# Optimization experiments

Measured on AMD Instinct MI355X. Metric: run time of the kernel, lower is better.

The kernel has to match this reference:

```python
import jax, jax.numpy as jnp
import numpy as np

T, B, H, I = 128, 32, 256, 256


def setup_inputs() -> dict:
    key = jax.random.key(0)
    ks = jax.random.split(key, 8)
    s = 0.05
    embs = jax.random.normal(ks[0], (T, B, I), jnp.float32)
    lens = jax.random.randint(ks[1], (B,), 1, T + 1)  # lengths in [1, T]
    W_ih = jax.random.normal(ks[2], (4 * H, I), jnp.float32) * s
    W_hh = jax.random.normal(ks[3], (4 * H, H), jnp.float32) * s
    b_ih = jax.random.normal(ks[4], (4 * H,), jnp.float32) * s
    b_hh = jax.random.normal(ks[5], (4 * H,), jnp.float32) * s
    W_a = jax.random.normal(ks[6], (H, 2 * H), jnp.float32) * s  # attention combine (Luong-style)
    b_a = jax.random.normal(ks[7], (H,), jnp.float32) * s
    return {"embs": embs, "lens": lens, "W_ih": W_ih, "W_hh": W_hh,
            "b_ih": b_ih, "b_hh": b_hh, "W_a": W_a, "b_a": b_a}


def reference(embs, lens, W_ih, W_hh, b_ih, b_hh, W_a, b_a):
    Tn, Bn, _ = embs.shape
    Hn = W_hh.shape[1]
    t_idx = jnp.arange(Tn)

    def step(carry, inp):
        h, c, buf, h_fin, c_fin = carry  # h,c: [B,H]; buf: [T,B,H] history of outputs
        t, emb = inp
        # dot-product attention of current hidden over past outputs (steps < t)
        scores = jnp.einsum('tbh,bh->tb', buf, h)
        valid = (t_idx < t)[:, None]
        alpha = jax.nn.softmax(jnp.where(valid, scores, -1e9), axis=0)
        ctx = jnp.einsum('tb,tbh->bh', alpha, buf)
        h_att = jnp.tanh(jnp.concatenate([ctx, h], axis=-1) @ W_a.T + b_a)
        h = jnp.where(t > 0, h_att, h)  # no history at t=0
        # standard PyTorch LSTM cell (gate order i,f,g,o)
        gates = emb @ W_ih.T + b_ih + h @ W_hh.T + b_hh
        i_g, f_g, g_g, o_g = jnp.split(gates, 4, axis=-1)
        c = jax.nn.sigmoid(f_g) * c + jax.nn.sigmoid(i_g) * jnp.tanh(g_g)
        h = jax.nn.sigmoid(o_g) * jnp.tanh(c)
        buf = buf.at[t].set(h)
        take = (t == lens - 1)[:, None]
        h_fin = jnp.where(take, h, h_fin)
        c_fin = jnp.where(take, c, c_fin)
        return (h, c, buf, h_fin, c_fin), h

    z = jnp.zeros((Bn, Hn), embs.dtype)
    buf0 = jnp.zeros((Tn, Bn, Hn), embs.dtype)
    carry, output = jax.lax.scan(step, (z, z, buf0, z, z), (t_idx, embs))
    # output: [T,B,H]; final (h,c) gathered at t == lens-1: [B,H]
    return output, carry[3], carry[4]
```

## Files before the change

### kernel.cpp

```cpp
#include <hip/hip_runtime.h>


#define T_DIM 128
#define B_DIM 32

typedef _Float16 half2_t __attribute__((ext_vector_type(2)));

static __device__ __forceinline__ unsigned pack2(float a, float b) {
  half2_t h;
  h.x = (_Float16)a;
  h.y = (_Float16)b;
  return __builtin_bit_cast(unsigned, h);
}

static __device__ __forceinline__ float dot2f(unsigned w, unsigned v, float acc) {
  half2_t a = __builtin_bit_cast(half2_t, w);
  half2_t b = __builtin_bit_cast(half2_t, v);
#if __has_builtin(__builtin_amdgcn_fdot2)
  return __builtin_amdgcn_fdot2(a, b, acc, false);
#else
  return acc + (float)a.x * (float)b.x + (float)a.y * (float)b.y;
#endif
}

static __device__ __forceinline__ float dot8(uint4 w, uint4 v, float acc) {
  acc = dot2f(w.x, v.x, acc);
  acc = dot2f(w.y, v.y, acc);
  acc = dot2f(w.z, v.z, acc);
  acc = dot2f(w.w, v.w, acc);
  return acc;
}

static __device__ __forceinline__ float lo16(unsigned u) {
  return (float)__builtin_bit_cast(half2_t, u).x;
}
static __device__ __forceinline__ float hi16(unsigned u) {
  return (float)__builtin_bit_cast(half2_t, u).y;
}

static __device__ __forceinline__ float fsig(float x) {
  return __builtin_amdgcn_rcpf(1.f + __expf(-x));
}
static __device__ __forceinline__ float ftanh(float x) {
  float e = __expf(2.f * x);
  return 1.f - 2.f * __builtin_amdgcn_rcpf(e + 1.f);
}

__global__ void pack_weights(const float* __restrict__ W_ih, const float* __restrict__ W_hh,
                             const float* __restrict__ W_a, float* __restrict__ W_ihT,
                             uint4* __restrict__ Whh_pack, uint4* __restrict__ Wa_pack,
                             unsigned long long* __restrict__ ywp,
                             unsigned long long* __restrict__ hx) {
  int n = blockIdx.x * 256 + threadIdx.x;
  {
    int k = n >> 10, r = n & 1023;
    W_ihT[n] = W_ih[r * 256 + k];
  }
  if (n < 32768) {
    int m = n >> 12, tid = (n >> 3) & 511, i = n & 7;
    int r_local = tid >> 2, qk = tid & 3;
    int q = r_local >> 5, jl = r_local & 31;
    int r = q * 256 + m * 32 + jl;
    const float* src = W_hh + r * 256 + (4 * i + qk) * 8;
    uint4 v;
    v.x = pack2(src[0], src[1]);
    v.y = pack2(src[2], src[3]);
    v.z = pack2(src[4], src[5]);
    v.w = pack2(src[6], src[7]);
    Whh_pack[n] = v;
  }
  if (n < 16384) {
    int m = n >> 11, thr = (n >> 2) & 511, c = n & 3;
    int j = thr >> 1, type = thr & 1;
    int col0 = type * 256 + m * 32 + c * 8;
    const float* src = W_a + j * 512 + col0;
    uint4 v;
    v.x = pack2(src[0], src[1]);
    v.y = pack2(src[2], src[3]);
    v.z = pack2(src[4], src[5]);
    v.w = pack2(src[6], src[7]);
    Wa_pack[n] = v;
  }
  if (n < 65536)
    __hip_atomic_store(&ywp[n], 0ull, __ATOMIC_RELAXED, __HIP_MEMORY_SCOPE_AGENT);
  else if (n < 69632)
    __hip_atomic_store(&hx[n - 65536], 0ull, __ATOMIC_RELAXED, __HIP_MEMORY_SCOPE_AGENT);
}

__global__ void compute_gih(const float* __restrict__ embs, const float* __restrict__ W_ihT,
                            const float* __restrict__ b_ih, const float* __restrict__ b_hh,
                            float* __restrict__ gih) {
  __shared__ float embS[8][256];
  const int tid = threadIdx.x;
  const int tb0 = blockIdx.x * 8;
#pragma unroll
  for (int e = 0; e < 8; ++e) embS[e][tid] = embs[(size_t)(tb0 + e) * 256 + tid];
  __syncthreads();
  float acc[8][4];
#pragma unroll
  for (int e = 0; e < 8; ++e)
#pragma unroll
    for (int q = 0; q < 4; ++q) acc[e][q] = 0.f;
  for (int k = 0; k < 256; ++k) {
    float w0 = W_ihT[k * 1024 + tid];
    float w1 = W_ihT[k * 1024 + tid + 256];
    float w2 = W_ihT[k * 1024 + tid + 512];
    float w3 = W_ihT[k * 1024 + tid + 768];
#pragma unroll
    for (int e = 0; e < 8; ++e) {
      float x = embS[e][k];
      acc[e][0] += x * w0;
      acc[e][1] += x * w1;
      acc[e][2] += x * w2;
      acc[e][3] += x * w3;
    }
  }
#pragma unroll
  for (int q = 0; q < 4; ++q) {
    float bias = b_ih[q * 256 + tid] + b_hh[q * 256 + tid];
#pragma unroll
    for (int e = 0; e < 8; ++e)
      gih[(size_t)(tb0 + e) * 1024 + q * 256 + tid] = acc[e][q] + bias;
  }
}

__global__ void __launch_bounds__(512, 1)
alstm_rec(const int* __restrict__ lens, const float* __restrict__ gih,
          const uint4* __restrict__ Whh_pack, const uint4* __restrict__ Wa_pack,
          const float* __restrict__ b_a, unsigned long long* __restrict__ hx,
          unsigned long long* __restrict__ ywp, float* __restrict__ out,
          float* __restrict__ hfin, float* __restrict__ cfin) {
  const int tid = threadIdx.x;
  const int b = blockIdx.x & 31;
  const int m = blockIdx.x >> 5;

  __shared__ __align__(16) unsigned histS[16384];
  __shared__ __align__(16) unsigned ystoreS[16384];
  __shared__ __align__(16) unsigned h2[128];
  __shared__ __align__(16) unsigned hp2[128];
  __shared__ __align__(16) unsigned hsl2[16];
  __shared__ float sc[128];
  __shared__ float zpartF[4][256];
  __shared__ float gsl[128];

  uint4 wh4[8];
  {
    const uint4* p = Whh_pack + ((size_t)m * 512 + tid) * 8;
#pragma unroll
    for (int i = 0; i < 8; ++i) wh4[i] = p[i];
  }
  uint4 wa4[4];
  {
    const uint4* p = Wa_pack + ((size_t)m * 512 + tid) * 4;
#pragma unroll
    for (int i = 0; i < 4; ++i) wa4[i] = p[i];
  }
  const float ba_j = (tid < 256) ? b_a[tid] : 0.f;
  const int len_b = lens[b];
  const int r_local = tid >> 2, qk = tid & 3;
  const int gq = r_local >> 5, gjl = r_local & 31;

  if (tid < 128) hp2[tid] = 0u;
  float c_reg = 0.f;
  __syncthreads();

  for (int t = 0; t < T_DIM; ++t) {
    float gih_v = gih[((size_t)t * 32 + b) * 1024 + gq * 256 + m * 32 + gjl];
    float w_j = 0.f;

    if (t > 0) {
      if (tid < 256) {
        const unsigned long long* base = ywp + b * 2048 + tid;
        unsigned long long v[8];
        for (;;) {
          bool ok = true;
#pragma unroll
          for (int mm = 0; mm < 8; ++mm)
            v[mm] = __hip_atomic_load(base + mm * 256, __ATOMIC_RELAXED, __HIP_MEMORY_SCOPE_AGENT);
#pragma unroll
          for (int mm = 0; mm < 8; ++mm) ok &= ((unsigned)v[mm] == (unsigned)t);
          if (ok) break;
          __builtin_amdgcn_s_sleep(1);
        }
        float y = 0.f, w = 0.f;
#pragma unroll
        for (int mm = 0; mm < 8; ++mm) {
          unsigned pl = (unsigned)(v[mm] >> 32);
          y += lo16(pl);
          w += hi16(pl);
        }
        w_j = w;
        float yn = __shfl_xor(y, 1);
        if (!(tid & 1)) {
          const int p = tid >> 1, sx = (t - 1) & 31;
          ystoreS[(t - 1) * 128 + ((((p >> 2) ^ sx) << 2) | (p & 3))] = pack2(y, yn);
        }
      } else if (tid < 384) {
        const int p = tid - 256;
        unsigned long long v;
        for (;;) {
          v = __hip_atomic_load(&hx[b * 128 + p], __ATOMIC_RELAXED, __HIP_MEMORY_SCOPE_AGENT);
          if ((unsigned)v == (unsigned)t) break;
          __builtin_amdgcn_s_sleep(1);
        }
        unsigned pair = (unsigned)(v >> 32);
        h2[p] = pair;
        histS[(t - 1) * 128 + ((((p >> 2) ^ ((t - 1) & 31)) << 2) | (p & 3))] = pair;
      }
      __syncthreads();
      {
        const int s = tid >> 2, part = tid & 3;
        float a = 0.f;
        if (s < t) {
          const int sx = s & 31;
#pragma unroll
          for (int i = 0; i < 8; ++i) {
            const int c = 4 * i + part;
            uint4 hv = *(const uint4*)&histS[s * 128 + ((c ^ sx) << 2)];
            uint4 qv = *(const uint4*)&h2[c << 2];
            a = dot8(hv, qv, a);
          }
        }
        a += __shfl_xor(a, 1);
        a += __shfl_xor(a, 2);
        if (part == 0 && s < t) sc[s] = a;
      }
      __syncthreads();
      if (tid < 64) {
        float v0 = (tid < t) ? sc[tid] : -3.0e38f;
        float v1 = (tid + 64 < t) ? sc[tid + 64] : -3.0e38f;
        float mx = fmaxf(v0, v1);
#pragma unroll
        for (int off = 32; off >= 1; off >>= 1) mx = fmaxf(mx, __shfl_xor(mx, off));
        float e0 = (tid < t) ? __expf(v0 - mx) : 0.f;
        float e1 = (tid + 64 < t) ? __expf(v1 - mx) : 0.f;
        float sm = e0 + e1;
#pragma unroll
        for (int off = 32; off >= 1; off >>= 1) sm += __shfl_xor(sm, off);
        float inv = __builtin_amdgcn_rcpf(sm);
        sc[tid] = e0 * inv;
        sc[tid + 64] = e1 * inv;
      }
      __syncthreads();
      {
        const int sp = tid >> 7, p2 = tid & 127;
        float c0 = 0.f, c1 = 0.f;
        for (int s = sp; s < t; s += 4) {
          float al = sc[s];
          unsigned yv = ystoreS[s * 128 + ((((p2 >> 2) ^ (s & 31)) << 2) | (p2 & 3))];
          c0 += al * lo16(yv);
          c1 += al * hi16(yv);
        }
        zpartF[sp][2 * p2] = c0;
        zpartF[sp][2 * p2 + 1] = c1;
      }
      __syncthreads();
      if (tid < 256) {
        float z = zpartF[0][tid] + zpartF[1][tid] + zpartF[2][tid] + zpartF[3][tid];
        float hv = ftanh(ba_j + w_j + z);
        float o = __shfl_xor(hv, 1);
        if (!(tid & 1)) hp2[tid >> 1] = pack2(hv, o);
      }
      __syncthreads();
    }
    {
      float a = 0.f;
#pragma unroll
      for (int i = 0; i < 8; ++i) {
        const int c = 4 * i + qk;
        uint4 hv = *(const uint4*)&hp2[c << 2];
        a = dot8(wh4[i], hv, a);
      }
      a += __shfl_xor(a, 1);
      a += __shfl_xor(a, 2);
      if (qk == 0) gsl[r_local] = a + gih_v;
    }
    __syncthreads();
    if (tid < 32) {
      float ig = fsig(gsl[tid]);
      float fg = fsig(gsl[32 + tid]);
      float gg = ftanh(gsl[64 + tid]);
      float og = fsig(gsl[96 + tid]);
      float cn = fg * c_reg + ig * gg;
      float hn = og * ftanh(cn);
      c_reg = cn;
      out[((size_t)t * 32 + b) * 256 + m * 32 + tid] = hn;
      if (t == len_b - 1) {
        hfin[b * 256 + m * 32 + tid] = hn;
        cfin[b * 256 + m * 32 + tid] = cn;
      }
      float o = __shfl_xor(hn, 1);
      if (!(tid & 1)) {
        unsigned u = pack2(hn, o);
        hsl2[tid >> 1] = u;
        unsigned long long v =
            ((unsigned long long)u << 32) | (unsigned long long)(unsigned)(t + 1);
        __hip_atomic_store(&hx[b * 128 + m * 16 + (tid >> 1)], v, __ATOMIC_RELAXED,
                           __HIP_MEMORY_SCOPE_AGENT);
      }
    }
    __syncthreads();
    {
      float acc = 0.f;
#pragma unroll
      for (int c = 0; c < 4; ++c) {
        uint4 hv = *(const uint4*)&hsl2[c * 4];
        acc = dot8(wa4[c], hv, acc);
      }
      float other = __shfl_xor(acc, 1);
      if (!(tid & 1)) {
        unsigned long long v = ((unsigned long long)pack2(acc, other) << 32) |
                               (unsigned long long)(unsigned)(t + 1);
        __hip_atomic_store(&ywp[b * 2048 + m * 256 + (tid >> 1)], v, __ATOMIC_RELAXED,
                           __HIP_MEMORY_SCOPE_AGENT);
      }
    }
  }
}

extern "C" void kernel_launch(void* const* d_in, const int* in_sizes, int n_in,
                              void* d_out, int out_size, void* d_ws, size_t ws_size,
                              hipStream_t stream) {
  const float* embs = (const float*)d_in[0];
  const int* lens = (const int*)d_in[1];
  const float* W_ih = (const float*)d_in[2];
  const float* W_hh = (const float*)d_in[3];
  const float* b_ih = (const float*)d_in[4];
  const float* b_hh = (const float*)d_in[5];
  const float* W_a = (const float*)d_in[6];
  const float* b_a = (const float*)d_in[7];

  float* out = (float*)d_out;
  float* hfin = out + (size_t)T_DIM * B_DIM * 256;
  float* cfin = hfin + (size_t)B_DIM * 256;

  char* ws = (char*)d_ws;
  float* gih = (float*)ws;
  float* W_ihT = (float*)(ws + 16777216);
  uint4* Whh_pack = (uint4*)(ws + 17825792);
  uint4* Wa_pack = (uint4*)(ws + 18350080);
  unsigned long long* ywp = (unsigned long long*)(ws + 18612224);
  unsigned long long* hx = (unsigned long long*)(ws + 19136512);

  pack_weights<<<1024, 256, 0, stream>>>(W_ih, W_hh, W_a, W_ihT, Whh_pack, Wa_pack, ywp, hx);
  compute_gih<<<512, 256, 0, stream>>>(embs, W_ihT, b_ih, b_hh, gih);
  alstm_rec<<<256, 512, 0, stream>>>(lens, gih, Whh_pack, Wa_pack, b_a, hx, ywp, out, hfin,
                                     cfin);
}
```

Baseline: 623.3 us.

## Distribute attention scores across column-slice blocks and exchange partial scores

Each block now keeps only its own 32-column slice of the hidden history and computes partial attention scores against all past steps for that slice, publishing them through a global flag-tagged buffer. Consumers sum the eight partials instead of gathering the full hidden vector and recomputing full dot products over the whole history. The y projection history is kept in fp32 shared memory, and the W_a projection work is remapped so one thread computes both the y and w halves for a row. The aim is to cut shared-memory traffic and the per-step score loop, at the cost of a different cross-block exchange pattern and an extra barrier.

```diff
diff --git a/kernel.cpp b/kernel.cpp
--- a/kernel.cpp
+++ b/kernel.cpp
@@ -50,7 +50,7 @@
                              const float* __restrict__ W_a, float* __restrict__ W_ihT,
                              uint4* __restrict__ Whh_pack, uint4* __restrict__ Wa_pack,
                              unsigned long long* __restrict__ ywp,
-                             unsigned long long* __restrict__ hx) {
+                             unsigned long long* __restrict__ psx) {
   int n = blockIdx.x * 256 + threadIdx.x;
   {
     int k = n >> 10, r = n & 1023;
@@ -70,9 +70,8 @@
     Whh_pack[n] = v;
   }
   if (n < 16384) {
-    int m = n >> 11, thr = (n >> 2) & 511, c = n & 3;
-    int j = thr >> 1, type = thr & 1;
-    int col0 = type * 256 + m * 32 + c * 8;
+    int m = n >> 11, j = (n >> 3) & 255, c = n & 7;
+    int col0 = (c < 4) ? (m * 32 + c * 8) : (256 + m * 32 + (c - 4) * 8);
     const float* src = W_a + j * 512 + col0;
     uint4 v;
     v.x = pack2(src[0], src[1]);
@@ -83,8 +82,8 @@
   }
   if (n < 65536)
     __hip_atomic_store(&ywp[n], 0ull, __ATOMIC_RELAXED, __HIP_MEMORY_SCOPE_AGENT);
-  else if (n < 69632)
-    __hip_atomic_store(&hx[n - 65536], 0ull, __ATOMIC_RELAXED, __HIP_MEMORY_SCOPE_AGENT);
+  else if (n < 81920)
+    __hip_atomic_store(&psx[n - 65536], 0ull, __ATOMIC_RELAXED, __HIP_MEMORY_SCOPE_AGENT);
 }
 
 __global__ void compute_gih(const float* __restrict__ embs, const float* __restrict__ W_ihT,
@@ -127,20 +126,19 @@
 __global__ void __launch_bounds__(512, 1)
 alstm_rec(const int* __restrict__ lens, const float* __restrict__ gih,
           const uint4* __restrict__ Whh_pack, const uint4* __restrict__ Wa_pack,
-          const float* __restrict__ b_a, unsigned long long* __restrict__ hx,
-          unsigned long long* __restrict__ ywp, float* __restrict__ out,
+          const float* __restrict__ b_a, unsigned long long* __restrict__ ywp,
+          unsigned long long* __restrict__ psx, float* __restrict__ out,
           float* __restrict__ hfin, float* __restrict__ cfin) {
   const int tid = threadIdx.x;
   const int b = blockIdx.x & 31;
   const int m = blockIdx.x >> 5;
 
-  __shared__ __align__(16) unsigned histS[16384];
-  __shared__ __align__(16) unsigned ystoreS[16384];
-  __shared__ __align__(16) unsigned h2[128];
+  __shared__ __align__(16) unsigned histSl[128 * 18];
+  __shared__ __align__(16) float ystoreF[128 * 256];
   __shared__ __align__(16) unsigned hp2[128];
   __shared__ __align__(16) unsigned hsl2[16];
   __shared__ float sc[128];
-  __shared__ float zpartF[4][256];
+  __shared__ float zp[4][256];
   __shared__ float gsl[128];
 
   uint4 wh4[8];
@@ -149,11 +147,14 @@
 #pragma unroll
     for (int i = 0; i < 8; ++i) wh4[i] = p[i];
   }
-  uint4 wa4[4];
+  uint4 way[4], waw[4];
   {
-    const uint4* p = Wa_pack + ((size_t)m * 512 + tid) * 4;
-#pragma unroll
-    for (int i = 0; i < 4; ++i) wa4[i] = p[i];
+    const int j_pub = (tid - 128) & 255;
+    const uint4* p = Wa_pack + ((size_t)m * 256 + j_pub) * 8;
+#pragma unroll
+    for (int i = 0; i < 4; ++i) way[i] = p[i];
+#pragma unroll
+    for (int i = 0; i < 4; ++i) waw[i] = p[4 + i];
   }
   const float ba_j = (tid < 256) ? b_a[tid] : 0.f;
   const int len_b = lens[b];
@@ -190,40 +191,30 @@
           w += hi16(pl);
         }
         w_j = w;
-        float yn = __shfl_xor(y, 1);
-        if (!(tid & 1)) {
-          const int p = tid >> 1, sx = (t - 1) & 31;
-          ystoreS[(t - 1) * 128 + ((((p >> 2) ^ sx) << 2) | (p & 3))] = pack2(y, yn);
-        }
-      } else if (tid < 384) {
+        ystoreF[(t - 1) * 256 + tid] = y;
+      } else if (tid < 320) {
         const int p = tid - 256;
-        unsigned long long v;
+        const unsigned long long* base = psx + b * 512 + p;
+        unsigned long long v[8];
         for (;;) {
-          v = __hip_atomic_load(&hx[b * 128 + p], __ATOMIC_RELAXED, __HIP_MEMORY_SCOPE_AGENT);
-          if ((unsigned)v == (unsigned)t) break;
+          bool ok = true;
+#pragma unroll
+          for (int mm = 0; mm < 8; ++mm)
+            v[mm] = __hip_atomic_load(base + mm * 64, __ATOMIC_RELAXED, __HIP_MEMORY_SCOPE_AGENT);
+#pragma unroll
+          for (int mm = 0; mm < 8; ++mm) ok &= ((unsigned)v[mm] == (unsigned)t);
+          if (ok) break;
           __builtin_amdgcn_s_sleep(1);
         }
-        unsigned pair = (unsigned)(v >> 32);
-        h2[p] = pair;
-        histS[(t - 1) * 128 + ((((p >> 2) ^ ((t - 1) & 31)) << 2) | (p & 3))] = pair;
-      }
-      __syncthreads();
-      {
-        const int s = tid >> 2, part = tid & 3;
-        float a = 0.f;
-        if (s < t) {
-          const int sx = s & 31;
-#pragma unroll
-          for (int i = 0; i < 8; ++i) {
-            const int c = 4 * i + part;
-            uint4 hv = *(const uint4*)&histS[s * 128 + ((c ^ sx) << 2)];
-            uint4 qv = *(const uint4*)&h2[c << 2];
-            a = dot8(hv, qv, a);
-          }
-        }
-        a += __shfl_xor(a, 1);
-        a += __shfl_xor(a, 2);
-        if (part == 0 && s < t) sc[s] = a;
+        float s0 = 0.f, s1 = 0.f;
+#pragma unroll
+        for (int mm = 0; mm < 8; ++mm) {
+          unsigned pl = (unsigned)(v[mm] >> 32);
+          s0 += lo16(pl);
+          s1 += hi16(pl);
+        }
+        sc[2 * p] = s0;
+        sc[2 * p + 1] = s1;
       }
       __syncthreads();
       if (tid < 64) {
@@ -245,18 +236,19 @@
       {
         const int sp = tid >> 7, p2 = tid & 127;
         float c0 = 0.f, c1 = 0.f;
+        const float* yb = ystoreF + 2 * p2;
         for (int s = sp; s < t; s += 4) {
           float al = sc[s];
-          unsigned yv = ystoreS[s * 128 + ((((p2 >> 2) ^ (s & 31)) << 2) | (p2 & 3))];
-          c0 += al * lo16(yv);
-          c1 += al * hi16(yv);
-        }
-        zpartF[sp][2 * p2] = c0;
-        zpartF[sp][2 * p2 + 1] = c1;
+          float2 yv = *(const float2*)(yb + s * 256);
+          c0 += al * yv.x;
+          c1 += al * yv.y;
+        }
+        zp[sp][2 * p2] = c0;
+        zp[sp][2 * p2 + 1] = c1;
       }
       __syncthreads();
       if (tid < 256) {
-        float z = zpartF[0][tid] + zpartF[1][tid] + zpartF[2][tid] + zpartF[3][tid];
+        float z = zp[0][tid] + zp[1][tid] + zp[2][tid] + zp[3][tid];
         float hv = ftanh(ba_j + w_j + z);
         float o = __shfl_xor(hv, 1);
         if (!(tid & 1)) hp2[tid >> 1] = pack2(hv, o);
@@ -293,27 +285,39 @@
       if (!(tid & 1)) {
         unsigned u = pack2(hn, o);
         hsl2[tid >> 1] = u;
-        unsigned long long v =
-            ((unsigned long long)u << 32) | (unsigned long long)(unsigned)(t + 1);
-        __hip_atomic_store(&hx[b * 128 + m * 16 + (tid >> 1)], v, __ATOMIC_RELAXED,
+        histSl[t * 18 + (tid >> 1)] = u;
+      }
+    }
+    __syncthreads();
+    if (tid < 128) {
+      float a = 0.f;
+#pragma unroll
+      for (int k = 0; k < 8; ++k) {
+        uint2 hw = *(const uint2*)&histSl[tid * 18 + 2 * k];
+        uint2 qv = *(const uint2*)&hsl2[2 * k];
+        a = dot2f(hw.x, qv.x, a);
+        a = dot2f(hw.y, qv.y, a);
+      }
+      float o = __shfl_xor(a, 1);
+      if (!(tid & 1)) {
+        unsigned long long v = ((unsigned long long)pack2(a, o) << 32) |
+                               (unsigned long long)(unsigned)(t + 1);
+        __hip_atomic_store(&psx[b * 512 + m * 64 + (tid >> 1)], v, __ATOMIC_RELAXED,
                            __HIP_MEMORY_SCOPE_AGENT);
       }
-    }
-    __syncthreads();
-    {
-      float acc = 0.f;
+    } else if (tid < 384) {
+      const int j = tid - 128;
+      float ay = 0.f, aw = 0.f;
 #pragma unroll
       for (int c = 0; c < 4; ++c) {
         uint4 hv = *(const uint4*)&hsl2[c * 4];
-        acc = dot8(wa4[c], hv, acc);
-      }
-      float other = __shfl_xor(acc, 1);
-      if (!(tid & 1)) {
-        unsigned long long v = ((unsigned long long)pack2(acc, other) << 32) |
-                               (unsigned long long)(unsigned)(t + 1);
-        __hip_atomic_store(&ywp[b * 2048 + m * 256 + (tid >> 1)], v, __ATOMIC_RELAXED,
-                           __HIP_MEMORY_SCOPE_AGENT);
-      }
+        ay = dot8(way[c], hv, ay);
+        aw = dot8(waw[c], hv, aw);
+      }
+      unsigned long long v = ((unsigned long long)pack2(ay, aw) << 32) |
+                             (unsigned long long)(unsigned)(t + 1);
+      __hip_atomic_store(&ywp[b * 2048 + m * 256 + j], v, __ATOMIC_RELAXED,
+                         __HIP_MEMORY_SCOPE_AGENT);
     }
   }
 }
@@ -340,10 +344,10 @@
   uint4* Whh_pack = (uint4*)(ws + 17825792);
   uint4* Wa_pack = (uint4*)(ws + 18350080);
   unsigned long long* ywp = (unsigned long long*)(ws + 18612224);
-  unsigned long long* hx = (unsigned long long*)(ws + 19136512);
-
-  pack_weights<<<1024, 256, 0, stream>>>(W_ih, W_hh, W_a, W_ihT, Whh_pack, Wa_pack, ywp, hx);
+  unsigned long long* psx = (unsigned long long*)(ws + 19136512);
+
+  pack_weights<<<1024, 256, 0, stream>>>(W_ih, W_hh, W_a, W_ihT, Whh_pack, Wa_pack, ywp, psx);
   compute_gih<<<512, 256, 0, stream>>>(embs, W_ihT, b_ih, b_hh, gih);
-  alstm_rec<<<256, 512, 0, stream>>>(lens, gih, Whh_pack, Wa_pack, b_a, hx, ywp, out, hfin,
+  alstm_rec<<<256, 512, 0, stream>>>(lens, gih, Whh_pack, Wa_pack, b_a, ywp, psx, out, hfin,
                                      cfin);
 }
```

Result: faster. 564.0 us (-9.5%).
